# Optimization experiments

Measured on AMD Instinct MI355X. Metric: run time of the kernel, lower is better.

Reference implementation:

```python
import jax, jax.numpy as jnp
import numpy as np

ALPHA = 0.95  # EMA decay for cluster_frequency
DIM = 64
CODEBOOK_SIZE = 1024


def setup_inputs() -> dict:
    key = jax.random.key(0)
    k1, k2 = jax.random.split(key)
    x = jax.random.normal(k1, (16, 4096, DIM), dtype=jnp.float32)
    # codebook is a learned Parameter of shape [dim, codebook_size]
    codebook = jax.random.normal(k2, (DIM, CODEBOOK_SIZE), dtype=jnp.float32)  # init_scale=1.0
    cluster_frequency = jnp.ones((CODEBOOK_SIZE,), dtype=jnp.float32)  # registered buffer
    return {"x": x, "codebook": codebook, "cluster_frequency": cluster_frequency}


def reference(x, codebook, cluster_frequency):
    # --- quantize: squared-distance via expansion, then argmin over codebook ---
    dist = (
        jnp.sum(x * x, axis=-1, keepdims=True)
        - 2.0 * jnp.einsum("bld,dk->blk", x, codebook)
        + jnp.sum(codebook * codebook, axis=0)
    )
    codebook_index = jnp.argmin(dist, axis=-1)  # [B, L]

    # --- dequantize: embedding gather from codebook.T ---
    x_quantized = jnp.take(codebook.T, codebook_index, axis=0)  # [B, L, D]

    # commitment loss (x pulled toward frozen codes)
    inner_loss = jnp.mean((jax.lax.stop_gradient(x_quantized) - x) ** 2)
    # codebook loss (training path; codes pulled toward frozen inputs)
    codebook_loss = jnp.mean((x_quantized - jax.lax.stop_gradient(x)) ** 2)
    inner_loss = inner_loss + codebook_loss

    # --- update_codebook_count (no_grad buffer update): scatter-add histogram + EMA ---
    codebook_count = jnp.zeros((codebook.shape[1],), dtype=x.dtype).at[
        codebook_index.reshape(-1)
    ].add(1.0)
    new_cluster_frequency = jax.lax.stop_gradient(
        ALPHA * cluster_frequency + (1.0 - ALPHA) * codebook_count
    )

    # straight-through estimator
    x_quantized_st = x + jax.lax.stop_gradient(x_quantized - x)
    return x_quantized_st, codebook_index, inner_loss, new_cluster_frequency
```

## Files before the change

### kernel.cpp

```cpp
#include <hip/hip_runtime.h>

#define DIM 64
#define NCODE 1024

typedef __attribute__((ext_vector_type(8))) short bf16x8;
typedef __attribute__((ext_vector_type(4))) float f32x4;

#define WSO_SLOTS 0
#define WSO_COUNT 4100
#define WSO_MAX4  4112
#define WSO_CBN   4160


__device__ __forceinline__ unsigned short f2bf(float f) {
    unsigned u = __float_as_uint(f);
    unsigned r = (u + 0x7FFFu + ((u >> 16) & 1u)) >> 16;
    return (unsigned short)r;
}

__device__ __forceinline__ void gload16(const void* g, void* l) {
    __builtin_amdgcn_global_load_lds(
        (const __attribute__((address_space(1))) unsigned int*)g,
        (__attribute__((address_space(3))) unsigned int*)l, 16, 0, 0);
}

__global__ __launch_bounds__(256) void vq_prep(const float* __restrict__ cb,
                                               char* __restrict__ ws,
                                               char* __restrict__ cbt,
                                               float* __restrict__ cbT) {
    __shared__ float red[256];
    const int t = threadIdx.x;
    const int k = blockIdx.x * 256 + t;

    float cv[64];
#pragma unroll
    for (int d = 0; d < DIM; ++d) cv[d] = cb[d * NCODE + k];

    float s = 0.f;
#pragma unroll
    for (int d = 0; d < DIM; ++d) s = fmaf(cv[d], cv[d], s);

    ((float*)(ws + WSO_CBN))[k] = s;
    if (blockIdx.x == 0) ((float*)(ws + WSO_SLOTS))[t] = 0.f;

    unsigned short hi[64], lo[64];
#pragma unroll
    for (int d = 0; d < DIM; ++d) {
        unsigned short h = f2bf(cv[d]);
        float hf = __uint_as_float(((unsigned)h) << 16);
        hi[d] = h;
        lo[d] = f2bf(cv[d] - hf);
    }

    const int c = k >> 6, cc = k & 63, wv = cc >> 4, col = cc & 15;
    char* base = cbt + (size_t)(c * 4 + wv) * 4096;
#pragma unroll
    for (int g = 0; g < 4; ++g) {
        bf16x8 h0v, h1v, l0v, l1v;
#pragma unroll
        for (int e = 0; e < 8; ++e) {
            h0v[e] = (short)hi[g * 8 + e];
            h1v[e] = (short)hi[32 + g * 8 + e];
            l0v[e] = (short)lo[g * 8 + e];
            l1v[e] = (short)lo[32 + g * 8 + e];
        }
        const int off = (g * 16 + col) * 16;
        *(bf16x8*)(base + off)        = h0v;
        *(bf16x8*)(base + 1024 + off) = h1v;
        *(bf16x8*)(base + 2048 + off) = l0v;
        *(bf16x8*)(base + 3072 + off) = l1v;
    }

#pragma unroll
    for (int j = 0; j < 16; ++j) {
        float4 v = {cv[4 * j], cv[4 * j + 1], cv[4 * j + 2], cv[4 * j + 3]};
        *(float4*)(cbT + (size_t)k * 64 + 4 * j) = v;
    }

    red[t] = s;
    __syncthreads();
    for (int m = 128; m > 0; m >>= 1) {
        if (t < m) red[t] = fmaxf(red[t], red[t + m]);
        __syncthreads();
    }
    if (t == 0) {
        ((float*)(ws + WSO_MAX4))[blockIdx.x] = red[0];
        if (blockIdx.x == 0) *(int*)(ws + WSO_COUNT) = 0;
    }
}

__global__ __launch_bounds__(256, 3) void vq_mfma(const float* __restrict__ x,
                                                  const char* __restrict__ cbt,
                                                  char* __restrict__ ws,
                                                  unsigned short* __restrict__ list,
                                                  float* __restrict__ out_idx) {
    __shared__ __align__(16) char sm[20736];
    char*  bX    = sm;
    float* cbn_s = (float*)(sm + 16384);
    float* xx_s  = (float*)(sm + 20480);
    float* R1    = (float*)sm;
    float* R2v   = R1 + 128;
    int*   RIv   = (int*)(R2v + 128);
    int*   cntL  = (int*)(sm + 8192);

    const int t = threadIdx.x, w = t >> 6, lane = t & 63;
    const int rh = w & 1, ct = w >> 1;
    const int r0 = blockIdx.x * 64;

    const float* mb4 = (const float*)(ws + WSO_MAX4);
    const float maxcbn = fmaxf(fmaxf(mb4[0], mb4[1]), fmaxf(mb4[2], mb4[3]));

    gload16((const char*)(ws + WSO_CBN) + ((size_t)w * 64 + lane) * 16, (char*)cbn_s + w * 1024);

    {
        const int row = t >> 2, q = t & 3;
        const float4* xp = (const float4*)(x + (size_t)(r0 + row) * DIM + q * 16);
        float4 v0 = xp[0], v1 = xp[1], v2 = xp[2], v3 = xp[3];
        float p = 0.f;
        p = fmaf(v0.x, v0.x, p); p = fmaf(v0.y, v0.y, p); p = fmaf(v0.z, v0.z, p); p = fmaf(v0.w, v0.w, p);
        p = fmaf(v1.x, v1.x, p); p = fmaf(v1.y, v1.y, p); p = fmaf(v1.z, v1.z, p); p = fmaf(v1.w, v1.w, p);
        p = fmaf(v2.x, v2.x, p); p = fmaf(v2.y, v2.y, p); p = fmaf(v2.z, v2.z, p); p = fmaf(v2.w, v2.w, p);
        p = fmaf(v3.x, v3.x, p); p = fmaf(v3.y, v3.y, p); p = fmaf(v3.z, v3.z, p); p = fmaf(v3.w, v3.w, p);
        p += __shfl_xor(p, 1);
        p += __shfl_xor(p, 2);
        if (q == 0) xx_s[row] = p;

        float hv[16] = {v0.x, v0.y, v0.z, v0.w, v1.x, v1.y, v1.z, v1.w,
                        v2.x, v2.y, v2.z, v2.w, v3.x, v3.y, v3.z, v3.w};
        bf16x8 ph[2], pl[2];
#pragma unroll
        for (int h = 0; h < 2; ++h)
#pragma unroll
            for (int e = 0; e < 8; ++e) {
                float v = hv[h * 8 + e];
                unsigned short hb = f2bf(v);
                float hf = __uint_as_float(((unsigned)hb) << 16);
                ph[h][e] = (short)hb;
                pl[h][e] = (short)f2bf(v - hf);
            }
        const int sw = row & 7;
        char* base = bX + row * 256;
#pragma unroll
        for (int h = 0; h < 2; ++h) {
            int s3 = (2 * q + h) ^ sw;
            *(bf16x8*)(base + (s3 & 7) * 16)        = ph[h];
            *(bf16x8*)(base + (8 | (s3 & 7)) * 16)  = pl[h];
        }
    }
    __syncthreads();

    bf16x8 afh[2][2], afl[2][2];
#pragma unroll
    for (int rt = 0; rt < 2; ++rt)
#pragma unroll
        for (int kt = 0; kt < 2; ++kt) {
            int row = rh * 32 + rt * 16 + (lane & 15);
            int s3 = ((kt * 4 + (lane >> 4)) ^ (row & 7)) & 7;
            afh[rt][kt] = *(const bf16x8*)(bX + row * 256 + s3 * 16);
            afl[rt][kt] = *(const bf16x8*)(bX + row * 256 + (8 | s3) * 16);
        }

    const int cl = ct * 16 + (lane & 15);

    float m1[8], m2[8];
    int   mi[8];
#pragma unroll
    for (int s = 0; s < 8; ++s) { m1[s] = 3.4e38f; m2[s] = 3.4e38f; mi[s] = 0; }

    const char* pc = cbt + (size_t)ct * 4096 + (size_t)lane * 16;

    bf16x8 bh0 = *(const bf16x8*)(pc);
    bf16x8 bh1 = *(const bf16x8*)(pc + 1024);
    bf16x8 bl0 = *(const bf16x8*)(pc + 2048);
    bf16x8 bl1 = *(const bf16x8*)(pc + 3072);

#pragma unroll 1
    for (int c2 = 0; c2 < 32; ++c2) {
        const char* np = pc + 8192;
        bf16x8 nh0 = *(const bf16x8*)(np);
        bf16x8 nh1 = *(const bf16x8*)(np + 1024);
        bf16x8 nl0 = *(const bf16x8*)(np + 2048);
        bf16x8 nl1 = *(const bf16x8*)(np + 3072);

        const int kg = c2 * 32 + cl;
        const float cbnv = cbn_s[kg];

#pragma unroll
        for (int rt = 0; rt < 2; ++rt) {
            f32x4 z = {0.f, 0.f, 0.f, 0.f};
            z = __builtin_amdgcn_mfma_f32_16x16x32_bf16(afh[rt][0], bh0, z, 0, 0, 0);
            z = __builtin_amdgcn_mfma_f32_16x16x32_bf16(afh[rt][1], bh1, z, 0, 0, 0);
            z = __builtin_amdgcn_mfma_f32_16x16x32_bf16(afl[rt][0], bh0, z, 0, 0, 0);
            z = __builtin_amdgcn_mfma_f32_16x16x32_bf16(afl[rt][1], bh1, z, 0, 0, 0);
            z = __builtin_amdgcn_mfma_f32_16x16x32_bf16(afh[rt][0], bl0, z, 0, 0, 0);
            z = __builtin_amdgcn_mfma_f32_16x16x32_bf16(afh[rt][1], bl1, z, 0, 0, 0);
#pragma unroll
            for (int v = 0; v < 4; ++v) {
                const int s = rt * 4 + v;
                float dd = fmaf(-2.f, z[v], cbnv);
                bool lt = dd < m1[s];
                m2[s] = fminf(m2[s], fmaxf(m1[s], dd));
                m1[s] = fminf(m1[s], dd);
                mi[s] = lt ? kg : mi[s];
            }
        }
        pc = np;
        bh0 = nh0; bh1 = nh1; bl0 = nl0; bl1 = nl1;
    }

#pragma unroll
    for (int m = 1; m <= 8; m <<= 1) {
#pragma unroll
        for (int s = 0; s < 8; ++s) {
            float o1 = __shfl_xor(m1[s], m);
            float o2 = __shfl_xor(m2[s], m);
            int   oi = __shfl_xor(mi[s], m);
            float nm2 = fminf(fminf(m2[s], o2), fmaxf(m1[s], o1));
            bool tk = (o1 < m1[s]) || (o1 == m1[s] && oi < mi[s]);
            m1[s] = fminf(m1[s], o1);
            mi[s] = tk ? oi : mi[s];
            m2[s] = nm2;
        }
    }
    __syncthreads();
    if ((lane & 15) == 0) {
        const int gq = lane >> 4;
#pragma unroll
        for (int s = 0; s < 8; ++s) {
            const int row = rh * 32 + (s >> 2) * 16 + gq * 4 + (s & 3);
            R1[row * 2 + ct]  = m1[s];
            R2v[row * 2 + ct] = m2[s];
            RIv[row * 2 + ct] = mi[s];
        }
    }
    __syncthreads();

    bool flag = false;
    int  rr = 0;
    if (t < 128) {
        const int row = t >> 1, q = t & 1;
        float a1 = R1[row * 2 + q];
        float A2 = R2v[row * 2 + q];
        int   ai = RIv[row * 2 + q];
        {
            float o1 = __shfl_xor(a1, 1);
            float o2 = __shfl_xor(A2, 1);
            int   oi = __shfl_xor(ai, 1);
            float nm2 = fminf(fminf(A2, o2), fmaxf(a1, o1));
            bool tk = (o1 < a1) || (o1 == a1 && oi < ai);
            a1 = fminf(a1, o1);
            ai = tk ? oi : ai;
            A2 = nm2;
        }
        if (q == 0) {
            const int r = r0 + row;
            out_idx[r] = (float)ai;
            const float Bv = 1.5e-4f * sqrtf(xx_s[row] * maxcbn) + 2e-3f;
            flag = (A2 - a1 <= 2.f * Bv);
            rr = r;
        }
    }
    unsigned long long mk = __ballot(flag);
    const int wcnt = __popcll(mk);
    if (lane == 0) cntL[w] = wcnt;
    __syncthreads();
    if (t == 0) {
        int c0 = cntL[0], c1 = cntL[1], c2 = cntL[2], c3 = cntL[3];
        int tot = c0 + c1 + c2 + c3;
        int base = 0;
        if (tot) base = atomicAdd((int*)(ws + WSO_COUNT), tot);
        cntL[0] = base;
        cntL[1] = base + c0;
        cntL[2] = base + c0 + c1;
        cntL[3] = base + c0 + c1 + c2;
    }
    __syncthreads();
    if (flag) {
        const int off = __popcll(mk & ((1ull << lane) - 1ull));
        list[cntL[w] + off] = (unsigned short)rr;
    }
}

__global__ void vq_refine(const float* __restrict__ x,
                          const float* __restrict__ cb,
                          const char* __restrict__ ws,
                          const unsigned short* __restrict__ list,
                          float* __restrict__ out_idx) {
    const int N = *(const int*)(ws + WSO_COUNT);
    const float* cbn = (const float*)(ws + WSO_CBN);
    __shared__ float rowx[4][64];
    const int t = threadIdx.x, w = t >> 6, lane = t & 63;

    for (int base = blockIdx.x * 4; base < N; base += (int)gridDim.x * 4) {
        const int ii = base + w;
        const bool valid = ii < N;
        const int r = valid ? (int)list[ii] : (int)list[0];

        __syncthreads();
        const float xv = x[(size_t)r * DIM + lane];
        rowx[w][lane] = xv;
        float p = xv * xv;
#pragma unroll
        for (int m = 1; m < 64; m <<= 1) p += __shfl_xor(p, m);
        const float xx = p;
        __syncthreads();

        float xr[64];
#pragma unroll
        for (int d = 0; d < 64; ++d) xr[d] = rowx[w][d];

        float bd = 3.4e38f;
        int   bk = 0;
        for (int kb = 0; kb < NCODE; kb += 64) {
            float d0 = 0.f, d1 = 0.f, d2 = 0.f, d3 = 0.f;
            const float* cp = cb + kb + lane;
#pragma unroll
            for (int d = 0; d < 64; d += 4) {
                d0 = fmaf(xr[d + 0], cp[(d + 0) * NCODE], d0);
                d1 = fmaf(xr[d + 1], cp[(d + 1) * NCODE], d1);
                d2 = fmaf(xr[d + 2], cp[(d + 2) * NCODE], d2);
                d3 = fmaf(xr[d + 3], cp[(d + 3) * NCODE], d3);
            }
            const float dot = (d0 + d1) + (d2 + d3);
            const float dist = fmaf(-2.f, dot, xx) + cbn[kb + lane];
            const int k = kb + lane;
            if (dist < bd) { bd = dist; bk = k; }
        }
#pragma unroll
        for (int m = 1; m < 64; m <<= 1) {
            float od = __shfl_xor(bd, m);
            int   ok = __shfl_xor(bk, m);
            if (od < bd || (od == bd && ok < bk)) { bd = od; bk = ok; }
        }
        if (lane == 0 && valid) out_idx[r] = (float)bk;
    }
}

__global__ __launch_bounds__(256) void vq_hist(const float* __restrict__ idx_f,
                                               float* __restrict__ partials) {
    __shared__ int lh[1024];
    const int t = threadIdx.x;
    lh[t] = 0; lh[t + 256] = 0; lh[t + 512] = 0; lh[t + 768] = 0;
    __syncthreads();
    const int base = blockIdx.x * 2048;
#pragma unroll
    for (int i = 0; i < 8; ++i) {
        int k = (int)idx_f[base + i * 256 + t];
        atomicAdd(&lh[k], 1);
    }
    __syncthreads();
    float* P = partials + (size_t)blockIdx.x * 1024;
    P[t]       = (float)lh[t];
    P[t + 256] = (float)lh[t + 256];
    P[t + 512] = (float)lh[t + 512];
    P[t + 768] = (float)lh[t + 768];
}

__global__ __launch_bounds__(256) void vq_freq(const float* __restrict__ cf,
                                               const float* __restrict__ partials,
                                               float* __restrict__ out_freq) {
    const int k = blockIdx.x * 256 + threadIdx.x;
    float s = 0.f;
#pragma unroll
    for (int b = 0; b < 32; ++b) s += partials[(size_t)b * 1024 + k];
    out_freq[k] = 0.95f * cf[k] + 0.05f * s;
}

__global__ __launch_bounds__(256) void vq_epi_main(const float* __restrict__ x,
                                                   const float* __restrict__ cbT,
                                                   const float* __restrict__ idx_f,
                                                   float* __restrict__ out_xq,
                                                   char* __restrict__ ws) {
    __shared__ float lred[4];
    const int t = threadIdx.x;
    const int r_lin = blockIdx.x * 32 + (t >> 3);
    const int r = (r_lin < 1024) ? r_lin : r_lin + 1024;
    const int q8 = t & 7;
    const int k = (int)idx_f[r];

    const float4* cp = (const float4*)(cbT + (size_t)k * 64 + q8 * 8);
    const float4* xp = (const float4*)(x + (size_t)r * DIM + q8 * 8);
    float4* op = (float4*)(out_xq + (size_t)r * DIM + q8 * 8);

    float4 c0 = cp[0], c1 = cp[1];
    float4 x0 = xp[0], x1 = xp[1];
    float e0 = c0.x - x0.x, e1 = c0.y - x0.y, e2 = c0.z - x0.z, e3 = c0.w - x0.w;
    float e4 = c1.x - x1.x, e5 = c1.y - x1.y, e6 = c1.z - x1.z, e7 = c1.w - x1.w;
    float4 o0, o1;
    o0.x = x0.x + e0; o0.y = x0.y + e1; o0.z = x0.z + e2; o0.w = x0.w + e3;
    o1.x = x1.x + e4; o1.y = x1.y + e5; o1.z = x1.z + e6; o1.w = x1.w + e7;
    op[0] = o0; op[1] = o1;

    float lsum = 0.f;
    lsum = fmaf(e0, e0, lsum); lsum = fmaf(e1, e1, lsum);
    lsum = fmaf(e2, e2, lsum); lsum = fmaf(e3, e3, lsum);
    lsum = fmaf(e4, e4, lsum); lsum = fmaf(e5, e5, lsum);
    lsum = fmaf(e6, e6, lsum); lsum = fmaf(e7, e7, lsum);

#pragma unroll
    for (int off = 1; off < 64; off <<= 1) lsum += __shfl_xor(lsum, off);
    if ((t & 63) == 0) lred[t >> 6] = lsum;
    __syncthreads();
    if (t == 0)
        atomicAdd((float*)(ws + WSO_SLOTS) + (blockIdx.x & 255),
                  (lred[0] + lred[1]) + (lred[2] + lred[3]));
}

__global__ __launch_bounds__(256) void vq_epi_tail(const float* __restrict__ x,
                                                   const float* __restrict__ cb,
                                                   const float* __restrict__ idx_f,
                                                   float* __restrict__ out_xq,
                                                   char* __restrict__ ws) {
    __shared__ float lred[4];
    const int t = threadIdx.x;
    const int row = 1024 + blockIdx.x * 64 + (t >> 2), q = t & 3;
    const int k = (int)idx_f[row];
    const float4* xp = (const float4*)(x + (size_t)row * DIM + q * 16);
    float4* op = (float4*)(out_xq + (size_t)row * DIM + q * 16);
    float lsum = 0.f;
#pragma unroll
    for (int j = 0; j < 4; ++j) {
        float4 xv = xp[j];
        const int d0 = q * 16 + 4 * j;
        float q0 = cb[(d0 + 0) * NCODE + k];
        float q1 = cb[(d0 + 1) * NCODE + k];
        float q2 = cb[(d0 + 2) * NCODE + k];
        float q3 = cb[(d0 + 3) * NCODE + k];
        float e0 = q0 - xv.x, e1 = q1 - xv.y, e2 = q2 - xv.z, e3 = q3 - xv.w;
        float4 o;
        o.x = xv.x + e0; o.y = xv.y + e1; o.z = xv.z + e2; o.w = xv.w + e3;
        op[j] = o;
        lsum = fmaf(e0, e0, lsum); lsum = fmaf(e1, e1, lsum);
        lsum = fmaf(e2, e2, lsum); lsum = fmaf(e3, e3, lsum);
    }
#pragma unroll
    for (int off = 1; off < 64; off <<= 1) lsum += __shfl_xor(lsum, off);
    if ((t & 63) == 0) lred[t >> 6] = lsum;
    __syncthreads();
    if (t == 0)
        atomicAdd((float*)(ws + WSO_SLOTS) + blockIdx.x,
                  (lred[0] + lred[1]) + (lred[2] + lred[3]));
}

__global__ __launch_bounds__(256) void vq_loss(const char* __restrict__ ws,
                                               float* __restrict__ out_loss) {
    __shared__ float red[256];
    const int t = threadIdx.x;
    red[t] = ((const float*)(ws + WSO_SLOTS))[t];
    __syncthreads();
    for (int m = 128; m > 0; m >>= 1) {
        if (t < m) red[t] += red[t + m];
        __syncthreads();
    }
    if (t == 0) {
        float m = red[0] / 4194304.0f;
        out_loss[0] = m + m;
    }
}

extern "C" void kernel_launch(void* const* d_in, const int* in_sizes, int n_in,
                              void* d_out, int out_size, void* d_ws, size_t ws_size,
                              hipStream_t stream) {
    const float* x  = (const float*)d_in[0];
    const float* cb = (const float*)d_in[1];
    const float* cf = (const float*)d_in[2];

    float* out      = (float*)d_out;
    float* out_xq   = out;
    float* out_idx  = out + 4194304;
    float* out_loss = out + 4194304 + 65536;
    float* out_freq = out_loss + 1;

    char* ws = (char*)d_ws;

    char*           cbt   = (char*)d_out;
    float*          cbT   = (float*)((char*)d_out + 262144);
    unsigned short* list  = (unsigned short*)((char*)d_out + 524288);
    float*          parts = (float*)((char*)d_out + 524288);

    vq_prep    <<<4,    256, 0, stream>>>(cb, ws, cbt, cbT);
    vq_mfma    <<<1024, 256, 0, stream>>>(x, cbt, ws, list, out_idx);
    vq_refine  <<<2048, 256, 0, stream>>>(x, cb, ws, list, out_idx);
    vq_hist    <<<32,   256, 0, stream>>>(out_idx, parts);
    vq_freq    <<<4,    256, 0, stream>>>(cf, parts, out_freq);
    vq_epi_main<<<2016, 256, 0, stream>>>(x, cbT, out_idx, out_xq, ws);
    vq_epi_tail<<<16,   256, 0, stream>>>(x, cb, out_idx, out_xq, ws);
    vq_loss    <<<1,    256, 0, stream>>>(ws, out_loss);
}
```

Baseline: 91.33 us.

## Split refine work per row across four waves with packed atomicMin reduction

The refine kernel now splits each flagged row's 1024-code search into four 256-code quarters, each handled by a separate wave. The partial results are merged with a 64-bit atomicMin on an order-preserving float key packed with the index. The x row is broadcast through lane shuffles instead of shared memory, which removes the block-level syncs. A new unpack kernel writes the final indices, which adds a launch and the atomic traffic in exchange for more parallelism when few rows need refinement.

```diff
diff --git a/kernel.cpp b/kernel.cpp
--- a/kernel.cpp
+++ b/kernel.cpp
@@ -22,6 +22,11 @@
     __builtin_amdgcn_global_load_lds(
         (const __attribute__((address_space(1))) unsigned int*)g,
         (__attribute__((address_space(3))) unsigned int*)l, 16, 0, 0);
+}
+
+__device__ __forceinline__ unsigned fkey(float f) {
+    unsigned b = __float_as_uint(f);
+    return (b & 0x80000000u) ? ~b : (b | 0x80000000u);
 }
 
 __global__ __launch_bounds__(256) void vq_prep(const float* __restrict__ cb,
@@ -93,6 +98,7 @@
                                                   const char* __restrict__ cbt,
                                                   char* __restrict__ ws,
                                                   unsigned short* __restrict__ list,
+                                                  unsigned long long* __restrict__ minpack,
                                                   float* __restrict__ out_idx) {
     __shared__ __align__(16) char sm[20736];
     char*  bX    = sm;
@@ -277,49 +283,47 @@
     __syncthreads();
     if (flag) {
         const int off = __popcll(mk & ((1ull << lane) - 1ull));
-        list[cntL[w] + off] = (unsigned short)rr;
-    }
-}
-
-__global__ void vq_refine(const float* __restrict__ x,
-                          const float* __restrict__ cb,
-                          const char* __restrict__ ws,
-                          const unsigned short* __restrict__ list,
-                          float* __restrict__ out_idx) {
+        const int pos = cntL[w] + off;
+        list[pos] = (unsigned short)rr;
+        minpack[pos] = ~0ull;
+    }
+}
+
+__global__ __launch_bounds__(256) void vq_refine(const float* __restrict__ x,
+                                                 const float* __restrict__ cb,
+                                                 const char* __restrict__ ws,
+                                                 const unsigned short* __restrict__ list,
+                                                 unsigned long long* __restrict__ minpack) {
     const int N = *(const int*)(ws + WSO_COUNT);
     const float* cbn = (const float*)(ws + WSO_CBN);
-    __shared__ float rowx[4][64];
     const int t = threadIdx.x, w = t >> 6, lane = t & 63;
-
-    for (int base = blockIdx.x * 4; base < N; base += (int)gridDim.x * 4) {
-        const int ii = base + w;
-        const bool valid = ii < N;
-        const int r = valid ? (int)list[ii] : (int)list[0];
-
-        __syncthreads();
+    const int gw = blockIdx.x * 4 + w;
+    const int items = N * 4;
+
+    for (int item = gw; item < items; item += 8192) {
+        const int i  = item >> 2;
+        const int qq = item & 3;
+        const int r  = (int)list[i];
+
         const float xv = x[(size_t)r * DIM + lane];
-        rowx[w][lane] = xv;
         float p = xv * xv;
 #pragma unroll
         for (int m = 1; m < 64; m <<= 1) p += __shfl_xor(p, m);
         const float xx = p;
-        __syncthreads();
-
-        float xr[64];
-#pragma unroll
-        for (int d = 0; d < 64; ++d) xr[d] = rowx[w][d];
 
         float bd = 3.4e38f;
         int   bk = 0;
-        for (int kb = 0; kb < NCODE; kb += 64) {
+#pragma unroll
+        for (int b = 0; b < 4; ++b) {
+            const int kb = qq * 256 + b * 64;
+            const float* cp = cb + kb + lane;
             float d0 = 0.f, d1 = 0.f, d2 = 0.f, d3 = 0.f;
-            const float* cp = cb + kb + lane;
-#pragma unroll
-            for (int d = 0; d < 64; d += 4) {
-                d0 = fmaf(xr[d + 0], cp[(d + 0) * NCODE], d0);
-                d1 = fmaf(xr[d + 1], cp[(d + 1) * NCODE], d1);
-                d2 = fmaf(xr[d + 2], cp[(d + 2) * NCODE], d2);
-                d3 = fmaf(xr[d + 3], cp[(d + 3) * NCODE], d3);
+#pragma unroll
+            for (int j = 0; j < 16; ++j) {
+                d0 = fmaf(__shfl(xv, 4 * j + 0), cp[(4 * j + 0) * NCODE], d0);
+                d1 = fmaf(__shfl(xv, 4 * j + 1), cp[(4 * j + 1) * NCODE], d1);
+                d2 = fmaf(__shfl(xv, 4 * j + 2), cp[(4 * j + 2) * NCODE], d2);
+                d3 = fmaf(__shfl(xv, 4 * j + 3), cp[(4 * j + 3) * NCODE], d3);
             }
             const float dot = (d0 + d1) + (d2 + d3);
             const float dist = fmaf(-2.f, dot, xx) + cbn[kb + lane];
@@ -332,8 +336,20 @@
             int   ok = __shfl_xor(bk, m);
             if (od < bd || (od == bd && ok < bk)) { bd = od; bk = ok; }
         }
-        if (lane == 0 && valid) out_idx[r] = (float)bk;
-    }
+        if (lane == 0) {
+            unsigned long long pk = ((unsigned long long)fkey(bd) << 32) | (unsigned)bk;
+            atomicMin(&minpack[i], pk);
+        }
+    }
+}
+
+__global__ __launch_bounds__(256) void vq_unpack(const char* __restrict__ ws,
+                                                 const unsigned short* __restrict__ list,
+                                                 const unsigned long long* __restrict__ minpack,
+                                                 float* __restrict__ out_idx) {
+    const int N = *(const int*)(ws + WSO_COUNT);
+    const int i = blockIdx.x * 256 + threadIdx.x;
+    if (i < N) out_idx[(int)list[i]] = (float)(unsigned)(minpack[i] & 0xFFFFFFFFull);
 }
 
 __global__ __launch_bounds__(256) void vq_hist(const float* __restrict__ idx_f,
@@ -473,14 +489,16 @@
 
     char* ws = (char*)d_ws;
 
-    char*           cbt   = (char*)d_out;
-    float*          cbT   = (float*)((char*)d_out + 262144);
-    unsigned short* list  = (unsigned short*)((char*)d_out + 524288);
-    float*          parts = (float*)((char*)d_out + 524288);
+    char*               cbt     = (char*)d_out;
+    float*              cbT     = (float*)((char*)d_out + 262144);
+    unsigned short*     list    = (unsigned short*)((char*)d_out + 524288);
+    float*              parts   = (float*)((char*)d_out + 524288);
+    unsigned long long* minpack = (unsigned long long*)((char*)d_out + 655360);
 
     vq_prep    <<<4,    256, 0, stream>>>(cb, ws, cbt, cbT);
-    vq_mfma    <<<1024, 256, 0, stream>>>(x, cbt, ws, list, out_idx);
-    vq_refine  <<<2048, 256, 0, stream>>>(x, cb, ws, list, out_idx);
+    vq_mfma    <<<1024, 256, 0, stream>>>(x, cbt, ws, list, minpack, out_idx);
+    vq_refine  <<<2048, 256, 0, stream>>>(x, cb, ws, list, minpack);
+    vq_unpack  <<<256,  256, 0, stream>>>(ws, list, minpack, out_idx);
     vq_hist    <<<32,   256, 0, stream>>>(out_idx, parts);
     vq_freq    <<<4,    256, 0, stream>>>(cf, parts, out_freq);
     vq_epi_main<<<2016, 256, 0, stream>>>(x, cbT, out_idx, out_xq, ws);
```

New measurement: 81.30 us, median of 2. -11.0%, faster.
